# Optimization experiments

Hardware: AMD Instinct MI355X
Metric: run time of the kernel (lower is better)

## Reference

```python
import jax, jax.numpy as jnp
import numpy as np

B, T = 2, 2048
N_EMBD_A, N_EMBD_B = 2048, 1024
N_EMBD_ATT, N_HEAD = 2048, 16
HEAD_SIZE = N_EMBD_ATT // N_HEAD  # 128
ROPE_BASE = 500000
INIT_STD = 0.02


def _rope_cache(seq_len, n_elem, base):
    theta = 1.0 / (base ** (jnp.arange(0, n_elem, 2, dtype=jnp.float32) / n_elem))
    idx_theta = jnp.outer(jnp.arange(seq_len, dtype=jnp.float32), theta)
    idx_theta = jnp.concatenate([idx_theta, idx_theta], axis=-1)  # repeat(1,2)
    return jnp.cos(idx_theta), jnp.sin(idx_theta)


def _apply_rope(x, cos, sin):
    # x: [B, H, T, hs]; cos/sin: [T, hs] broadcast over batch and heads
    h = x.shape[-1]
    x1, x2 = x[..., : h // 2], x[..., h // 2 :]
    rotated = jnp.concatenate([-x2, x1], axis=-1)
    return x * cos[None, None] + rotated * sin[None, None]


def setup_inputs() -> dict:
    key = jax.random.key(0)
    k = jax.random.split(key, 6)
    Na = B * T // 2
    x_a = jax.random.normal(k[0], (Na, N_EMBD_A), jnp.float32)
    x_b = jax.random.normal(k[1], (B * T - Na, N_EMBD_B), jnp.float32)
    cos, sin = _rope_cache(T, HEAD_SIZE, ROPE_BASE)
    # alternating stream assignment: even positions -> stream a
    mask_a = (jnp.arange(B * T) % 2 == 0).reshape(B, T)
    Wa = INIT_STD * jax.random.normal(k[2], (N_EMBD_A, 3 * N_EMBD_ATT), jnp.float32)
    Wb = INIT_STD * jax.random.normal(k[3], (N_EMBD_B, 3 * N_EMBD_ATT), jnp.float32)
    Wpa = INIT_STD * jax.random.normal(k[4], (N_EMBD_ATT, N_EMBD_A), jnp.float32)
    Wpb = INIT_STD * jax.random.normal(k[5], (N_EMBD_ATT, N_EMBD_B), jnp.float32)
    return {"x_a": x_a, "x_b": x_b, "cos": cos, "sin": sin, "mask_a": mask_a,
            "Wa": Wa, "Wb": Wb, "Wpa": Wpa, "Wpb": Wpb}


def reference(x_a, x_b, cos, sin, mask_a, Wa, Wb, Wpa, Wpb):
    Na = x_a.shape[0]
    Bm, Tm = mask_a.shape
    qkv_a = x_a @ Wa  # [Na, 3*C]
    qkv_b = x_b @ Wb  # [Nb, 3*C]
    # interleave_tokens: scatter a-tokens into True positions, b-tokens into False
    mask_flat = mask_a.reshape(-1)
    # stable sort: indices of True positions first (in order), then False positions
    perm = jnp.argsort(jnp.logical_not(mask_flat), stable=True)  # [B*T]
    interleaved = jnp.zeros((Bm * Tm, qkv_a.shape[-1]), qkv_a.dtype)
    interleaved = interleaved.at[perm].set(jnp.concatenate([qkv_a, qkv_b], axis=0))
    kqv = interleaved.reshape(Bm, Tm, 3 * N_HEAD, HEAD_SIZE).transpose(0, 2, 1, 3)
    q, k, v = (kqv[:, :N_HEAD], kqv[:, N_HEAD:2 * N_HEAD], kqv[:, 2 * N_HEAD:])
    q = _apply_rope(q, cos, sin)
    k = _apply_rope(k, cos, sin)
    # causal SDPA
    scale = 1.0 / jnp.sqrt(jnp.float32(HEAD_SIZE))
    scores = jnp.einsum('bhqd,bhkd->bhqk', q, k) * scale  # [B,H,T,T]
    causal = jnp.tril(jnp.ones((Tm, Tm), bool))
    scores = jnp.where(causal, scores, jnp.float32(-1e30))
    att = jax.nn.softmax(scores, axis=-1)
    y = jnp.einsum('bhqk,bhkd->bhqd', att, v)
    y = y.transpose(0, 2, 1, 3).reshape(Bm * Tm, N_EMBD_ATT)
    # gather per-stream rows (row-major True/False order == perm order)
    y_sorted = y[perm]
    y_a = y_sorted[:Na] @ Wpa
    y_b = y_sorted[Na:] @ Wpb
    return y_a, y_b
```

## Files before the change

kernel.cpp:

```cpp
#include <hip/hip_runtime.h>


#define GLOBAL_AS __attribute__((address_space(1)))
#define LDS_AS    __attribute__((address_space(3)))

typedef unsigned short ushort8_t __attribute__((ext_vector_type(8)));
typedef unsigned short ushort4_t __attribute__((ext_vector_type(4)));
typedef unsigned int   uint4_t   __attribute__((ext_vector_type(4)));
typedef __bf16 bf16x8   __attribute__((ext_vector_type(8)));
typedef float  f32x4    __attribute__((ext_vector_type(4)));
typedef float  f32x16   __attribute__((ext_vector_type(16)));

__device__ __forceinline__ unsigned short f2bf(float f) {
  unsigned u = __builtin_bit_cast(unsigned, f);
  u += 0x7fffu + ((u >> 16) & 1u);
  return (unsigned short)(u >> 16);
}
__device__ __forceinline__ float bf2f(unsigned short h) {
  return __builtin_bit_cast(float, (unsigned)h << 16);
}
__device__ __forceinline__ bf16x8 ld_bf8(const unsigned short* p) {
  return __builtin_bit_cast(bf16x8, *reinterpret_cast<const ushort8_t*>(p));
}

__global__ void cast_bf16_kernel(const float* __restrict__ in,
                                 unsigned short* __restrict__ out, int n4) {
  int i = blockIdx.x * blockDim.x + threadIdx.x;
  if (i >= n4) return;
  float4 v = reinterpret_cast<const float4*>(in)[i];
  ushort4_t o;
  o[0] = f2bf(v.x); o[1] = f2bf(v.y); o[2] = f2bf(v.z); o[3] = f2bf(v.w);
  reinterpret_cast<ushort4_t*>(out)[i] = o;
}

__global__ void tcast_kernel(const float* __restrict__ in,
                             unsigned short* __restrict__ out, int R, int C) {
  __shared__ float t[32][33];
  int tx = threadIdx.x, ty = threadIdx.y;
  int r0 = blockIdx.y * 32, c0 = blockIdx.x * 32;
#pragma unroll
  for (int i = 0; i < 32; i += 8)
    t[ty + i][tx] = in[(size_t)(r0 + ty + i) * C + (c0 + tx)];
  __syncthreads();
#pragma unroll
  for (int i = 0; i < 32; i += 8)
    out[(size_t)(c0 + ty + i) * R + (r0 + tx)] = f2bf(t[tx][ty + i]);
}

template <bool OUT_BF16>
__global__ __launch_bounds__(256, 2)
void gemm_bt_kernel(const unsigned short* __restrict__ A, int lda, int a_stride,
                    const unsigned short* __restrict__ Bt, int ldb,
                    void* __restrict__ Cp, int ldc, int c_stride, int c_off,
                    int K) {
  __shared__ __align__(16) unsigned short As[128 * 32];
  __shared__ __align__(16) unsigned short Bs[128 * 32];
  const int tid = threadIdx.x;
  const int l = tid & 63, w = tid >> 6;
  const int lr = l & 15, g = l >> 4;
  const int wr = w >> 1, wc = w & 1;
  const int nwg = gridDim.x * gridDim.y;
  const int flat = blockIdx.y * gridDim.x + blockIdx.x;
  const int swz = (flat & 7) * (nwg >> 3) + (flat >> 3);
  const int m0 = (swz / gridDim.x) * 128, n0 = (swz % gridDim.x) * 128;

  f32x4 acc[4][4] = {};

  auto stage = [&](int k0) {
#pragma unroll
    for (int p = 0; p < 2; ++p) {
      int q = p * 256 + tid;
      int row = q >> 2;
      int col = (q & 3) * 8;
      unsigned lds_off = (unsigned)(p * 256 + w * 64) * 16u;
      const unsigned short* ga =
          A + ((size_t)(m0 + row) * a_stride) * lda + (k0 + col);
      __builtin_amdgcn_global_load_lds((GLOBAL_AS void*)ga,
                                       (LDS_AS void*)((char*)As + lds_off),
                                       16, 0, 0);
      const unsigned short* gb = Bt + (size_t)(n0 + row) * ldb + (k0 + col);
      __builtin_amdgcn_global_load_lds((GLOBAL_AS void*)gb,
                                       (LDS_AS void*)((char*)Bs + lds_off),
                                       16, 0, 0);
    }
  };

  stage(0);
  const int nk = K >> 5;
  for (int kt = 0; kt < nk; ++kt) {
    __syncthreads();
    bf16x8 aF[4], bF[4];
#pragma unroll
    for (int m = 0; m < 4; ++m)
      aF[m] = ld_bf8(&As[(wr * 64 + m * 16 + lr) * 32 + g * 8]);
#pragma unroll
    for (int n = 0; n < 4; ++n)
      bF[n] = ld_bf8(&Bs[(wc * 64 + n * 16 + lr) * 32 + g * 8]);
#pragma unroll
    for (int m = 0; m < 4; ++m)
#pragma unroll
      for (int n = 0; n < 4; ++n)
        acc[m][n] = __builtin_amdgcn_mfma_f32_16x16x32_bf16(aF[m], bF[n],
                                                            acc[m][n], 0, 0, 0);
    __syncthreads();
    if (kt + 1 < nk) stage((kt + 1) * 32);
  }

#pragma unroll
  for (int m = 0; m < 4; ++m) {
#pragma unroll
    for (int n = 0; n < 4; ++n) {
      int c = n0 + wc * 64 + n * 16 + lr;
#pragma unroll
      for (int i = 0; i < 4; ++i) {
        int r = m0 + wr * 64 + m * 16 + g * 4 + i;
        size_t off = (size_t)(r * c_stride + c_off) * ldc + c;
        if (OUT_BF16)
          ((unsigned short*)Cp)[off] = f2bf(acc[m][n][i]);
        else
          ((float*)Cp)[off] = acc[m][n][i];
      }
    }
  }
}

__global__ void rope_kernel(unsigned short* __restrict__ qkv,
                            const float* __restrict__ cosp,
                            const float* __restrict__ sinp) {
  int idx = blockIdx.x * blockDim.x + threadIdx.x;
  int d = idx & 63;
  int h2 = (idx >> 6) & 31;
  int row = idx >> 11;
  int t = row & 2047;
  unsigned short* base = qkv + (size_t)row * 6144 + h2 * 128;
  float x1 = bf2f(base[d]);
  float x2 = bf2f(base[d + 64]);
  float c = cosp[t * 128 + d];
  float s = sinp[t * 128 + d];
  base[d]      = f2bf(x1 * c - x2 * s);
  base[d + 64] = f2bf(x2 * c + x1 * s);
}

__global__ __launch_bounds__(256, 2)
void attn_kernel(const unsigned short* __restrict__ qkv,
                 unsigned short* __restrict__ y) {
  __shared__ __align__(16) unsigned short Vt[2][128][40];
  const int tid = threadIdx.x;
  const int l = tid & 63, w = tid >> 6;
  const int l31 = l & 31, hi = l >> 5;
  const int bh = blockIdx.x & 31, qt = blockIdx.x >> 5;
  const int b = bh >> 4, h = bh & 15;
  const int q0b = qt * 128;
  const int q0w = q0b + w * 32;
  const int qg = q0w + l31;
  const unsigned short* qbase = qkv + (size_t)b * 2048 * 6144 + h * 128;
  const unsigned short* kbase = qbase + 2048;
  const unsigned short* vbase = qbase + 4096;
  const float scale = 0.08838834764831845f;

  bf16x8 qB[8];
#pragma unroll
  for (int c = 0; c < 8; ++c)
    qB[c] = ld_bf8(qbase + (size_t)qg * 6144 + c * 16 + hi * 8);

  f32x16 o[4] = {};
  float m = -__builtin_inff(), lsum = 0.f;

  const int skv = tid & 31;
  const int sd0 = (tid >> 5) * 4;
  ushort4_t vr[4];
  auto vload = [&](int kv0) {
#pragma unroll
    for (int p = 0; p < 4; ++p)
      vr[p] = *reinterpret_cast<const ushort4_t*>(
          vbase + (size_t)(kv0 + skv) * 6144 + sd0 + p * 32);
  };
  auto vstore = [&](int buf) {
#pragma unroll
    for (int p = 0; p < 4; ++p)
#pragma unroll
      for (int j = 0; j < 4; ++j)
        Vt[buf][sd0 + p * 32 + j][skv] = vr[p][j];
  };

  const int nt = (q0b + 128) >> 5;
  const int ntw = ((q0w + 32) >> 5);
  vload(0);
  vstore(0);
  if (nt > 1) vload(32);
  __syncthreads();

  int cur = 0;
  for (int t = 0; t < nt; ++t) {
    const int kv0 = t * 32;
    if (t + 1 < nt) {
      vstore(cur ^ 1);
      if (t + 2 < nt) vload(kv0 + 64);
    }

    if (t < ntw) {
      f32x16 sA = {};
      __builtin_amdgcn_s_setprio(1);
#pragma unroll
      for (int c = 0; c < 8; ++c) {
        bf16x8 kf =
            ld_bf8(kbase + (size_t)(kv0 + l31) * 6144 + c * 16 + hi * 8);
        sA = __builtin_amdgcn_mfma_f32_32x32x16_bf16(kf, qB[c], sA, 0, 0, 0);
      }
      __builtin_amdgcn_s_setprio(0);

      float pmax = -1e30f;
#pragma unroll
      for (int r = 0; r < 16; ++r) {
        int kvg = kv0 + (r & 3) + 8 * (r >> 2) + 4 * hi;
        float v = sA[r] * scale;
        v = (kvg > qg) ? -1e30f : v;
        sA[r] = v;
        pmax = fmaxf(pmax, v);
      }
      pmax = fmaxf(pmax, __shfl_xor(pmax, 32, 64));

      if (!__all(pmax <= m + 8.f)) {
        float mn = fmaxf(m, pmax);
        float scv = __expf(m - mn);
        m = mn;
        lsum *= scv;
#pragma unroll
        for (int r = 0; r < 16; ++r) {
          int crow = (r & 3) + 8 * (r >> 2) + 4 * hi;
          float sr = __shfl(scv, crow, 64);
          o[0][r] *= sr; o[1][r] *= sr; o[2][r] *= sr; o[3][r] *= sr;
        }
      }

      float psum = 0.f;
#pragma unroll
      for (int r = 0; r < 16; ++r) {
        float pr = __expf(sA[r] - m);
        sA[r] = pr;
        psum += pr;
      }
      psum += __shfl_xor(psum, 32, 64);
      lsum += psum;

      unsigned wd[8];
#pragma unroll
      for (int k = 0; k < 8; ++k)
        wd[k] = (unsigned)f2bf(sA[2 * k]) |
                ((unsigned)f2bf(sA[2 * k + 1]) << 16);
      uint4_t paw0, paw1;
      {
        unsigned xs = (unsigned)__shfl_xor((int)wd[0], 32, 64);
        unsigned ys = (unsigned)__shfl_xor((int)wd[2], 32, 64);
        paw0[0] = hi ? ys : wd[0];
        paw0[2] = hi ? wd[2] : xs;
        xs = (unsigned)__shfl_xor((int)wd[1], 32, 64);
        ys = (unsigned)__shfl_xor((int)wd[3], 32, 64);
        paw0[1] = hi ? ys : wd[1];
        paw0[3] = hi ? wd[3] : xs;
        xs = (unsigned)__shfl_xor((int)wd[4], 32, 64);
        ys = (unsigned)__shfl_xor((int)wd[6], 32, 64);
        paw1[0] = hi ? ys : wd[4];
        paw1[2] = hi ? wd[6] : xs;
        xs = (unsigned)__shfl_xor((int)wd[5], 32, 64);
        ys = (unsigned)__shfl_xor((int)wd[7], 32, 64);
        paw1[1] = hi ? ys : wd[5];
        paw1[3] = hi ? wd[7] : xs;
      }
      bf16x8 pa0 = __builtin_bit_cast(bf16x8, paw0);
      bf16x8 pa1 = __builtin_bit_cast(bf16x8, paw1);

      __builtin_amdgcn_s_setprio(1);
#pragma unroll
      for (int n = 0; n < 4; ++n) {
        bf16x8 vb0 = ld_bf8(&Vt[cur][n * 32 + l31][hi * 8]);
        bf16x8 vb1 = ld_bf8(&Vt[cur][n * 32 + l31][16 + hi * 8]);
        o[n] = __builtin_amdgcn_mfma_f32_32x32x16_bf16(pa0, vb0, o[n], 0, 0, 0);
        o[n] = __builtin_amdgcn_mfma_f32_32x32x16_bf16(pa1, vb1, o[n], 0, 0, 0);
      }
      __builtin_amdgcn_s_setprio(0);
    }

    __syncthreads();
    cur ^= 1;
  }

  float linv = 1.f / lsum;
#pragma unroll
  for (int r = 0; r < 16; ++r) {
    int crow = (r & 3) + 8 * (r >> 2) + 4 * hi;
    float li = __shfl(linv, crow, 64);
    size_t base = (size_t)(b * 2048 + q0w + crow) * 2048 + h * 128 + l31;
    y[base +  0] = f2bf(o[0][r] * li);
    y[base + 32] = f2bf(o[1][r] * li);
    y[base + 64] = f2bf(o[2][r] * li);
    y[base + 96] = f2bf(o[3][r] * li);
  }
}

extern "C" void kernel_launch(void* const* d_in, const int* in_sizes, int n_in,
                              void* d_out, int out_size, void* d_ws,
                              size_t ws_size, hipStream_t stream) {
  const float* x_a  = (const float*)d_in[0];
  const float* x_b  = (const float*)d_in[1];
  const float* cosp = (const float*)d_in[2];
  const float* sinp = (const float*)d_in[3];
  const float* Wa   = (const float*)d_in[5];
  const float* Wb   = (const float*)d_in[6];
  const float* Wpa  = (const float*)d_in[7];
  const float* Wpb  = (const float*)d_in[8];
  float* out = (float*)d_out;

  const size_t MB = 1024 * 1024;
  char* ws = (char*)d_ws;
  unsigned short* qkvb = (unsigned short*)(ws + 0);
  unsigned short* WaT  = (unsigned short*)(ws + 48 * MB);
  unsigned short* yb   = (unsigned short*)(ws + 48 * MB);
  unsigned short* WbT  = (unsigned short*)(ws + 72 * MB);
  unsigned short* xa_bf= (unsigned short*)(ws + 84 * MB);
  unsigned short* WpaT = (unsigned short*)(ws + 84 * MB);
  unsigned short* xb_bf= (unsigned short*)(ws + 92 * MB);
  unsigned short* WpbT = (unsigned short*)(ws + 92 * MB);

  cast_bf16_kernel<<<4096, 256, 0, stream>>>(x_a, xa_bf, 2048 * 2048 / 4);
  cast_bf16_kernel<<<2048, 256, 0, stream>>>(x_b, xb_bf, 2048 * 1024 / 4);
  tcast_kernel<<<dim3(192, 64), dim3(32, 8), 0, stream>>>(Wa, WaT, 2048, 6144);
  tcast_kernel<<<dim3(192, 32), dim3(32, 8), 0, stream>>>(Wb, WbT, 1024, 6144);
  gemm_bt_kernel<true><<<dim3(48, 16), 256, 0, stream>>>(
      xa_bf, 2048, 1, WaT, 2048, qkvb, 6144, 2, 0, 2048);
  gemm_bt_kernel<true><<<dim3(48, 16), 256, 0, stream>>>(
      xb_bf, 1024, 1, WbT, 1024, qkvb, 6144, 2, 1, 1024);
  tcast_kernel<<<dim3(64, 64),  dim3(32, 8), 0, stream>>>(Wpa, WpaT, 2048, 2048);
  tcast_kernel<<<dim3(32, 64),  dim3(32, 8), 0, stream>>>(Wpb, WpbT, 2048, 1024);
  rope_kernel<<<32768, 256, 0, stream>>>(qkvb, cosp, sinp);
  attn_kernel<<<512, 256, 0, stream>>>(qkvb, yb);
  gemm_bt_kernel<false><<<dim3(16, 16), 256, 0, stream>>>(
      yb, 2048, 2, WpaT, 2048, out, 2048, 1, 0, 2048);
  gemm_bt_kernel<false><<<dim3(8, 16), 256, 0, stream>>>(
      yb + 2048, 2048, 2, WpbT, 2048, out + (size_t)2048 * 2048, 1024, 1, 0,
      2048);
}
```

Measured before the change: 555.7 us.

## Batch paired GEMMs into single launches, prefetch K tiles, and reorder attention blocks

```diff
diff --git a/kernel.cpp b/kernel.cpp
--- a/kernel.cpp
+++ b/kernel.cpp
@@ -47,22 +47,26 @@
     out[(size_t)(c0 + ty + i) * R + (r0 + tx)] = f2bf(t[tx][ty + i]);
 }
 
+struct GArg {
+  const unsigned short* A; int lda; int a_stride;
+  const unsigned short* Bt; int ldb;
+  void* Cp; int ldc; int c_stride; int c_off;
+  int K; int ntiles; int nwg;
+};
+
 template <bool OUT_BF16>
 __global__ __launch_bounds__(256, 2)
-void gemm_bt_kernel(const unsigned short* __restrict__ A, int lda, int a_stride,
-                    const unsigned short* __restrict__ Bt, int ldb,
-                    void* __restrict__ Cp, int ldc, int c_stride, int c_off,
-                    int K) {
+void gemm_bt_kernel(GArg g0, GArg g1, int split) {
+  const GArg& g = ((int)blockIdx.x < split) ? g0 : g1;
+  int flat = ((int)blockIdx.x < split) ? blockIdx.x : blockIdx.x - split;
   __shared__ __align__(16) unsigned short As[128 * 32];
   __shared__ __align__(16) unsigned short Bs[128 * 32];
   const int tid = threadIdx.x;
   const int l = tid & 63, w = tid >> 6;
-  const int lr = l & 15, g = l >> 4;
+  const int lr = l & 15, gq = l >> 4;
   const int wr = w >> 1, wc = w & 1;
-  const int nwg = gridDim.x * gridDim.y;
-  const int flat = blockIdx.y * gridDim.x + blockIdx.x;
-  const int swz = (flat & 7) * (nwg >> 3) + (flat >> 3);
-  const int m0 = (swz / gridDim.x) * 128, n0 = (swz % gridDim.x) * 128;
+  const int swz = (flat & 7) * (g.nwg >> 3) + (flat >> 3);
+  const int m0 = (swz / g.ntiles) * 128, n0 = (swz % g.ntiles) * 128;
 
   f32x4 acc[4][4] = {};
 
@@ -74,11 +78,11 @@
       int col = (q & 3) * 8;
       unsigned lds_off = (unsigned)(p * 256 + w * 64) * 16u;
       const unsigned short* ga =
-          A + ((size_t)(m0 + row) * a_stride) * lda + (k0 + col);
+          g.A + ((size_t)(m0 + row) * g.a_stride) * g.lda + (k0 + col);
       __builtin_amdgcn_global_load_lds((GLOBAL_AS void*)ga,
                                        (LDS_AS void*)((char*)As + lds_off),
                                        16, 0, 0);
-      const unsigned short* gb = Bt + (size_t)(n0 + row) * ldb + (k0 + col);
+      const unsigned short* gb = g.Bt + (size_t)(n0 + row) * g.ldb + (k0 + col);
       __builtin_amdgcn_global_load_lds((GLOBAL_AS void*)gb,
                                        (LDS_AS void*)((char*)Bs + lds_off),
                                        16, 0, 0);
@@ -86,16 +90,16 @@
   };
 
   stage(0);
-  const int nk = K >> 5;
+  const int nk = g.K >> 5;
   for (int kt = 0; kt < nk; ++kt) {
     __syncthreads();
     bf16x8 aF[4], bF[4];
 #pragma unroll
     for (int m = 0; m < 4; ++m)
-      aF[m] = ld_bf8(&As[(wr * 64 + m * 16 + lr) * 32 + g * 8]);
+      aF[m] = ld_bf8(&As[(wr * 64 + m * 16 + lr) * 32 + gq * 8]);
 #pragma unroll
     for (int n = 0; n < 4; ++n)
-      bF[n] = ld_bf8(&Bs[(wc * 64 + n * 16 + lr) * 32 + g * 8]);
+      bF[n] = ld_bf8(&Bs[(wc * 64 + n * 16 + lr) * 32 + gq * 8]);
 #pragma unroll
     for (int m = 0; m < 4; ++m)
 #pragma unroll
@@ -113,12 +117,12 @@
       int c = n0 + wc * 64 + n * 16 + lr;
 #pragma unroll
       for (int i = 0; i < 4; ++i) {
-        int r = m0 + wr * 64 + m * 16 + g * 4 + i;
-        size_t off = (size_t)(r * c_stride + c_off) * ldc + c;
+        int r = m0 + wr * 64 + m * 16 + gq * 4 + i;
+        size_t off = (size_t)(r * g.c_stride + g.c_off) * g.ldc + c;
         if (OUT_BF16)
-          ((unsigned short*)Cp)[off] = f2bf(acc[m][n][i]);
+          ((unsigned short*)g.Cp)[off] = f2bf(acc[m][n][i]);
         else
-          ((float*)Cp)[off] = acc[m][n][i];
+          ((float*)g.Cp)[off] = acc[m][n][i];
       }
     }
   }
@@ -148,7 +152,8 @@
   const int tid = threadIdx.x;
   const int l = tid & 63, w = tid >> 6;
   const int l31 = l & 31, hi = l >> 5;
-  const int bh = blockIdx.x & 31, qt = blockIdx.x >> 5;
+  const int bh = blockIdx.x & 31;
+  const int qt = 15 - (blockIdx.x >> 5);
   const int b = bh >> 4, h = bh & 15;
   const int q0b = qt * 128;
   const int q0w = q0b + w * 32;
@@ -156,7 +161,7 @@
   const unsigned short* qbase = qkv + (size_t)b * 2048 * 6144 + h * 128;
   const unsigned short* kbase = qbase + 2048;
   const unsigned short* vbase = qbase + 4096;
-  const float scale = 0.08838834764831845f;
+  const float scale2 = 0.08838834764831845f * 1.4426950408889634f;
 
   bf16x8 qB[8];
 #pragma unroll
@@ -164,7 +169,7 @@
     qB[c] = ld_bf8(qbase + (size_t)qg * 6144 + c * 16 + hi * 8);
 
   f32x16 o[4] = {};
-  float m = -__builtin_inff(), lsum = 0.f;
+  float m = -1e30f, lsum = 0.f;
 
   const int skv = tid & 31;
   const int sd0 = (tid >> 5) * 4;
@@ -183,46 +188,51 @@
         Vt[buf][sd0 + p * 32 + j][skv] = vr[p][j];
   };
 
+  auto kload = [&](bf16x8 (&kn)[8], int kv0) {
+#pragma unroll
+    for (int c = 0; c < 8; ++c)
+      kn[c] = ld_bf8(kbase + (size_t)(kv0 + l31) * 6144 + c * 16 + hi * 8);
+  };
+
   const int nt = (q0b + 128) >> 5;
-  const int ntw = ((q0w + 32) >> 5);
+  const int ntw = (q0w + 32) >> 5;
+  bf16x8 kA[8], kB[8];
   vload(0);
   vstore(0);
   if (nt > 1) vload(32);
+  kload(kA, 0);
   __syncthreads();
 
-  int cur = 0;
-  for (int t = 0; t < nt; ++t) {
+  auto body = [&](int t, int buf, bf16x8 (&kc)[8], bf16x8 (&kn)[8]) {
     const int kv0 = t * 32;
     if (t + 1 < nt) {
-      vstore(cur ^ 1);
+      vstore(buf ^ 1);
       if (t + 2 < nt) vload(kv0 + 64);
     }
-
     if (t < ntw) {
+      if (t + 1 < ntw) kload(kn, kv0 + 32);
+
       f32x16 sA = {};
       __builtin_amdgcn_s_setprio(1);
 #pragma unroll
-      for (int c = 0; c < 8; ++c) {
-        bf16x8 kf =
-            ld_bf8(kbase + (size_t)(kv0 + l31) * 6144 + c * 16 + hi * 8);
-        sA = __builtin_amdgcn_mfma_f32_32x32x16_bf16(kf, qB[c], sA, 0, 0, 0);
-      }
+      for (int c = 0; c < 8; ++c)
+        sA = __builtin_amdgcn_mfma_f32_32x32x16_bf16(kc[c], qB[c], sA, 0, 0, 0);
       __builtin_amdgcn_s_setprio(0);
 
       float pmax = -1e30f;
 #pragma unroll
       for (int r = 0; r < 16; ++r) {
         int kvg = kv0 + (r & 3) + 8 * (r >> 2) + 4 * hi;
-        float v = sA[r] * scale;
+        float v = sA[r] * scale2;
         v = (kvg > qg) ? -1e30f : v;
         sA[r] = v;
         pmax = fmaxf(pmax, v);
       }
       pmax = fmaxf(pmax, __shfl_xor(pmax, 32, 64));
 
-      if (!__all(pmax <= m + 8.f)) {
+      if (!__all(pmax <= m + 11.5f)) {
         float mn = fmaxf(m, pmax);
-        float scv = __expf(m - mn);
+        float scv = exp2f(m - mn);
         m = mn;
         lsum *= scv;
 #pragma unroll
@@ -236,7 +246,7 @@
       float psum = 0.f;
 #pragma unroll
       for (int r = 0; r < 16; ++r) {
-        float pr = __expf(sA[r] - m);
+        float pr = exp2f(sA[r] - m);
         sA[r] = pr;
         psum += pr;
       }
@@ -273,16 +283,19 @@
       __builtin_amdgcn_s_setprio(1);
 #pragma unroll
       for (int n = 0; n < 4; ++n) {
-        bf16x8 vb0 = ld_bf8(&Vt[cur][n * 32 + l31][hi * 8]);
-        bf16x8 vb1 = ld_bf8(&Vt[cur][n * 32 + l31][16 + hi * 8]);
+        bf16x8 vb0 = ld_bf8(&Vt[buf][n * 32 + l31][hi * 8]);
+        bf16x8 vb1 = ld_bf8(&Vt[buf][n * 32 + l31][16 + hi * 8]);
         o[n] = __builtin_amdgcn_mfma_f32_32x32x16_bf16(pa0, vb0, o[n], 0, 0, 0);
         o[n] = __builtin_amdgcn_mfma_f32_32x32x16_bf16(pa1, vb1, o[n], 0, 0, 0);
       }
       __builtin_amdgcn_s_setprio(0);
     }
-
     __syncthreads();
-    cur ^= 1;
+  };
+
+  for (int t = 0; t < nt; t += 2) {
+    body(t, 0, kA, kB);
+    body(t + 1, 1, kB, kA);
   }
 
   float linv = 1.f / lsum;
@@ -326,17 +339,19 @@
   cast_bf16_kernel<<<2048, 256, 0, stream>>>(x_b, xb_bf, 2048 * 1024 / 4);
   tcast_kernel<<<dim3(192, 64), dim3(32, 8), 0, stream>>>(Wa, WaT, 2048, 6144);
   tcast_kernel<<<dim3(192, 32), dim3(32, 8), 0, stream>>>(Wb, WbT, 1024, 6144);
-  gemm_bt_kernel<true><<<dim3(48, 16), 256, 0, stream>>>(
-      xa_bf, 2048, 1, WaT, 2048, qkvb, 6144, 2, 0, 2048);
-  gemm_bt_kernel<true><<<dim3(48, 16), 256, 0, stream>>>(
-      xb_bf, 1024, 1, WbT, 1024, qkvb, 6144, 2, 1, 1024);
+  {
+    GArg ga = {xa_bf, 2048, 1, WaT, 2048, qkvb, 6144, 2, 0, 2048, 48, 768};
+    GArg gb = {xb_bf, 1024, 1, WbT, 1024, qkvb, 6144, 2, 1, 1024, 48, 768};
+    gemm_bt_kernel<true><<<1536, 256, 0, stream>>>(ga, gb, 768);
+  }
   tcast_kernel<<<dim3(64, 64),  dim3(32, 8), 0, stream>>>(Wpa, WpaT, 2048, 2048);
   tcast_kernel<<<dim3(32, 64),  dim3(32, 8), 0, stream>>>(Wpb, WpbT, 2048, 1024);
   rope_kernel<<<32768, 256, 0, stream>>>(qkvb, cosp, sinp);
   attn_kernel<<<512, 256, 0, stream>>>(qkvb, yb);
-  gemm_bt_kernel<false><<<dim3(16, 16), 256, 0, stream>>>(
-      yb, 2048, 2, WpaT, 2048, out, 2048, 1, 0, 2048);
-  gemm_bt_kernel<false><<<dim3(8, 16), 256, 0, stream>>>(
-      yb + 2048, 2048, 2, WpbT, 2048, out + (size_t)2048 * 2048, 1024, 1, 0,
-      2048);
-}
+  {
+    GArg ga = {yb, 2048, 2, WpaT, 2048, out, 2048, 1, 0, 2048, 16, 256};
+    GArg gb = {yb + 2048, 2048, 2, WpbT, 2048, out + (size_t)2048 * 2048, 1024,
+               1, 0, 2048, 8, 128};
+    gemm_bt_kernel<false><<<384, 256, 0, stream>>>(ga, gb, 256);
+  }
+}
```

New measurement: 495.8 us. 1.12x faster.
